# Optimization experiments

Measured on AMD Instinct MI355X. Metric: run time of the kernel, lower is better.

## Reference

```python
import jax, jax.numpy as jnp
import numpy as np

N_ROBOTS = 32   # len(cfg.ENV.WALKERS)
SEQ = 12        # cfg.MODEL.MAX_LIMBS
LOBS = 52       # per-limb proprioceptive obs size
HID = 256       # cfg.MODEL.MLP.HIDDEN_DIM
LOUT = 2        # out_dim // SEQ
BATCH = 1024


def _uniform(k, shape, r):
    return jax.random.uniform(k, shape, jnp.float32, -r, r)


def setup_inputs() -> dict:
    key = jax.random.key(0)
    ks = jax.random.split(key, 14)
    obs = jax.random.normal(ks[0], (BATCH, SEQ * LOBS), jnp.float32)
    obs_mask = jax.random.randint(ks[1], (BATCH, SEQ), 0, 2).astype(bool)
    unimal_ids = jax.random.randint(ks[2], (BATCH,), 0, N_ROBOTS).astype(jnp.int32)
    ir_in, ir = 0.04, 1.0 / 16
    return {
        "obs": obs,
        "obs_mask": obs_mask,
        "unimal_ids": unimal_ids,
        "Wi": _uniform(ks[3], (N_ROBOTS, SEQ, LOBS, HID), ir_in),
        "bi": _uniform(ks[4], (N_ROBOTS, SEQ, HID), ir_in / SEQ),
        "W1": _uniform(ks[5], (N_ROBOTS, HID, HID), ir),
        "b1": _uniform(ks[6], (N_ROBOTS, HID), ir),
        "W2": _uniform(ks[7], (N_ROBOTS, HID, HID), ir),
        "b2": _uniform(ks[8], (N_ROBOTS, HID), ir),
        "W3": _uniform(ks[9], (N_ROBOTS, HID, HID), ir),
        "b3": _uniform(ks[10], (N_ROBOTS, HID), ir),
        "Wo": _uniform(ks[11], (N_ROBOTS, SEQ, HID, LOUT), ir),
        "bo": _uniform(ks[12], (N_ROBOTS, SEQ, LOUT), ir),
    }


def reference(obs, obs_mask, unimal_ids, Wi, bi, W1, b1, W2, b2, W3, b3, Wo, bo):
    B = obs.shape[0]
    o3 = obs.reshape(B, SEQ, LOBS)
    # HN_INPUT branch: per-robot input hypernetwork weights
    emb = jnp.einsum("bsl,bslh->bsh", o3, Wi[unimal_ids]) + bi[unimal_ids]
    emb = emb * (1.0 - obs_mask.astype(emb.dtype))[:, :, None]
    emb = jax.nn.relu(emb.sum(axis=1))  # [B, HID]
    # PER_ROBOT_HIDDEN_LAYERS: three per-robot dense layers
    emb = jax.nn.relu(jnp.einsum("bh,bhk->bk", emb, W1[unimal_ids]) + b1[unimal_ids])
    emb = jax.nn.relu(jnp.einsum("bh,bhk->bk", emb, W2[unimal_ids]) + b2[unimal_ids])
    emb = jax.nn.relu(jnp.einsum("bh,bhk->bk", emb, W3[unimal_ids]) + b3[unimal_ids])
    # HN_OUTPUT branch: per-robot, per-limb output hypernetwork
    out = jnp.einsum("bh,bshd->bsd", emb, Wo[unimal_ids]) + bo[unimal_ids]
    return out.reshape(B, -1)  # [B, SEQ*LOUT]
```

## Files before the change

### kernel.cpp

```cpp
#include <hip/hip_runtime.h>

#define NROB 32
#define SEQ 12
#define LOBS 52
#define HID 256
#define LOUT 2
#define BATCH 1024
#define KIN 624
#define XROW 636
#define SPB 8
#define NSD 24
#define NBLK 320
#define SLOTS 40

__device__ __forceinline__ void fma4(float4& a, const float4 w, const float s) {
  a.x = fmaf(w.x, s, a.x);
  a.y = fmaf(w.y, s, a.y);
  a.z = fmaf(w.z, s, a.z);
  a.w = fmaf(w.w, s, a.w);
}

template <int ROWS, int XS>
__device__ __forceinline__ void stream8(const float* __restrict__ Wr,
                                        const float* Xb, float4* acc) {
  static_assert(ROWS % 8 == 0, "ROWS must be multiple of 8");
  constexpr int G = ROWS / 8;
  const float* wp = Wr;
  float4 a0 = *(const float4*)(wp);
  float4 a1 = *(const float4*)(wp + HID);
  float4 a2 = *(const float4*)(wp + 2 * HID);
  float4 a3 = *(const float4*)(wp + 3 * HID);
  wp += 4 * HID;
#pragma unroll
  for (int g = 0; g < G; ++g) {
    const int k = g * 8;
    const float4 b0 = *(const float4*)(wp);
    const float4 b1 = *(const float4*)(wp + HID);
    const float4 b2 = *(const float4*)(wp + 2 * HID);
    const float4 b3 = *(const float4*)(wp + 3 * HID);
    wp += 4 * HID;
#pragma unroll
    for (int m = 0; m < SPB; ++m) {
      const float4 x = *(const float4*)(Xb + m * XS + k);
      fma4(acc[m], a0, x.x);
      fma4(acc[m], a1, x.y);
      fma4(acc[m], a2, x.z);
      fma4(acc[m], a3, x.w);
    }
    if (g + 1 < G) {
      a0 = *(const float4*)(wp);
      a1 = *(const float4*)(wp + HID);
      a2 = *(const float4*)(wp + 2 * HID);
      a3 = *(const float4*)(wp + 3 * HID);
      wp += 4 * HID;
    }
#pragma unroll
    for (int m = 0; m < SPB; ++m) {
      const float4 x = *(const float4*)(Xb + m * XS + k + 4);
      fma4(acc[m], b0, x.x);
      fma4(acc[m], b1, x.y);
      fma4(acc[m], b2, x.z);
      fma4(acc[m], b3, x.w);
    }
  }
}

__global__ __launch_bounds__(512, 4) void k_fused(
    const float* __restrict__ obs, const int* __restrict__ mask,
    const int* __restrict__ ids, const float* __restrict__ Wi,
    const float* __restrict__ bi, const float* __restrict__ W1,
    const float* __restrict__ b1, const float* __restrict__ W2,
    const float* __restrict__ b2, const float* __restrict__ W3,
    const float* __restrict__ b3, const float* __restrict__ Wo,
    const float* __restrict__ bo, float* __restrict__ out) {
  __shared__ int s_cnt[NROB];
  __shared__ int s_wc[16];
  __shared__ int s_bm[SPB], s_vm[SPB], s_mb[SPB];
  __shared__ __align__(16) float s_x0[SPB * XROW];
  __shared__ __align__(16) float s_P[4][SPB][HID];
  __shared__ __align__(16) float s_x1[SPB][HID];

  const int t = threadIdx.x;
  const int bx = blockIdx.x;

  if (t < NROB) s_cnt[t] = 0;
  if (t < SPB) s_bm[t] = 0;
  __syncthreads();
  const int id0 = ids[t];
  const int id1 = ids[t + 512];
  atomicAdd(&s_cnt[id0], 1);
  atomicAdd(&s_cnt[id1], 1);
  __syncthreads();

  int myr = -1, mybase = 0;
  {
    int maxbucket = 0;
    for (int x = 0; x < 8; ++x) {
      int bsum = 0;
      for (int r = x; r < NROB; r += 8) bsum += (s_cnt[r] + SPB - 1) >> 3;
      maxbucket = max(maxbucket, bsum);
    }
    if (maxbucket <= SLOTS) {
      const int myxcd = bx & 7, myslot = bx >> 3;
      int slot = 0;
      for (int r = myxcd; r < NROB; r += 8) {
        const int nch = (s_cnt[r] + SPB - 1) >> 3;
        if (myr < 0 && myslot >= slot && myslot < slot + nch) {
          myr = r;
          mybase = (myslot - slot) * SPB;
        }
        slot += nch;
      }
    } else {
      int ch = 0;
      for (int r = 0; r < NROB; ++r) {
        const int nch = (s_cnt[r] + SPB - 1) >> 3;
        if (myr < 0 && bx >= ch && bx < ch + nch) {
          myr = r;
          mybase = (bx - ch) * SPB;
        }
        ch += nch;
      }
    }
  }
  if (myr < 0) return;
  const int mycnt = s_cnt[myr];

  {
    const int wv = t >> 6;
    const unsigned lane = t & 63;
    const unsigned long long m0 = __ballot(id0 == myr);
    const unsigned long long m1 = __ballot(id1 == myr);
    if (lane == 0) {
      s_wc[wv] = __popcll(m0);
      s_wc[8 + wv] = __popcll(m1);
    }
    __syncthreads();
    const unsigned long long below = (1ull << lane) - 1ull;
    int pre0 = 0;
    for (int i = 0; i < wv; ++i) pre0 += s_wc[i];
    if (id0 == myr) {
      const int j = pre0 + __popcll(m0 & below) - mybase;
      if (j >= 0 && j < SPB) s_bm[j] = t;
    }
    int pre1 = 0;
    for (int i = 0; i < 8 + wv; ++i) pre1 += s_wc[i];
    if (id1 == myr) {
      const int j = pre1 + __popcll(m1 & below) - mybase;
      if (j >= 0 && j < SPB) s_bm[j] = t + 512;
    }
    __syncthreads();
  }
  if (t < SPB) {
    const int v = (mybase + t) < mycnt;
    s_vm[t] = v;
    int mb = 0xFFF;
    if (v) {
      mb = 0;
      const int b = s_bm[t];
      for (int s = 0; s < SEQ; ++s) mb |= (mask[b * SEQ + s] != 0) << s;
    }
    s_mb[t] = mb;
  }
  __syncthreads();

  for (int q = t; q < SPB * (KIN / 4); q += 512) {
    const int m = q / 156, f4 = q - m * 156;
    const int s = f4 / 13;
    float4 v = {0.f, 0.f, 0.f, 0.f};
    if (!((s_mb[m] >> s) & 1))
      v = *(const float4*)(obs + (size_t)s_bm[m] * KIN + f4 * 4);
    *(float4*)&s_x0[m * XROW + f4 * 4] = v;
  }
  if (t < SPB * SEQ) {
    const int m = t / SEQ, s = t - m * SEQ;
    s_x0[m * XROW + KIN + s] = ((s_mb[m] >> s) & 1) ? 0.f : 1.f;
  }
  __syncthreads();

  const int w = t >> 6, lane = t & 63;

  {
    float4 acc[SPB];
#pragma unroll
    for (int m = 0; m < SPB; ++m) acc[m] = {0.f, 0.f, 0.f, 0.f};
    const float* Wr = Wi + ((size_t)myr * KIN + w * 80) * HID + lane * 4;
    if (w < 7)
      stream8<80, XROW>(Wr, &s_x0[w * 80], acc);
    else
      stream8<64, XROW>(Wr, &s_x0[w * 80], acc);
    float* Pp = &s_P[w >> 1][0][lane * 4];
    if ((w & 1) == 0) {
#pragma unroll
      for (int m = 0; m < SPB; ++m) *(float4*)(Pp + m * HID) = acc[m];
    }
    __syncthreads();
    if (w & 1) {
#pragma unroll
      for (int m = 0; m < SPB; ++m) {
        float4 c = *(const float4*)(Pp + m * HID);
        c.x += acc[m].x;
        c.y += acc[m].y;
        c.z += acc[m].z;
        c.w += acc[m].w;
        *(float4*)(Pp + m * HID) = c;
      }
    }
    __syncthreads();
    {
      const int m = t >> 6, c4 = (t & 63) * 4;
      const float4 p0 = *(const float4*)&s_P[0][m][c4];
      const float4 p1 = *(const float4*)&s_P[1][m][c4];
      const float4 p2 = *(const float4*)&s_P[2][m][c4];
      const float4 p3 = *(const float4*)&s_P[3][m][c4];
      float4 a = {p0.x + p1.x + p2.x + p3.x, p0.y + p1.y + p2.y + p3.y,
                  p0.z + p1.z + p2.z + p3.z, p0.w + p1.w + p2.w + p3.w};
      const float* br = bi + (size_t)myr * SEQ * HID + c4;
#pragma unroll
      for (int s = 0; s < SEQ; ++s)
        fma4(a, *(const float4*)(br + s * HID), s_x0[m * XROW + KIN + s]);
      float4 o = {fmaxf(a.x, 0.f), fmaxf(a.y, 0.f), fmaxf(a.z, 0.f),
                  fmaxf(a.w, 0.f)};
      *(float4*)&s_x1[m][c4] = o;
    }
    __syncthreads();
  }

  float* X2 = s_x0;
  const float* Ws[3] = {W1, W2, W3};
  const float* bs[3] = {b1, b2, b3};
#pragma unroll
  for (int L = 0; L < 3; ++L) {
    const float* Xin = (L & 1) ? X2 : &s_x1[0][0];
    float* Xout = (L & 1) ? &s_x1[0][0] : X2;
    float4 acc[SPB];
#pragma unroll
    for (int m = 0; m < SPB; ++m) acc[m] = {0.f, 0.f, 0.f, 0.f};
    const float* Wr = Ws[L] + ((size_t)myr * HID + w * 32) * HID + lane * 4;
    stream8<32, HID>(Wr, Xin + w * 32, acc);
    float* Pp = &s_P[w >> 1][0][lane * 4];
    if ((w & 1) == 0) {
#pragma unroll
      for (int m = 0; m < SPB; ++m) *(float4*)(Pp + m * HID) = acc[m];
    }
    __syncthreads();
    if (w & 1) {
#pragma unroll
      for (int m = 0; m < SPB; ++m) {
        float4 c = *(const float4*)(Pp + m * HID);
        c.x += acc[m].x;
        c.y += acc[m].y;
        c.z += acc[m].z;
        c.w += acc[m].w;
        *(float4*)(Pp + m * HID) = c;
      }
    }
    __syncthreads();
    {
      const int m = t >> 6, c4 = (t & 63) * 4;
      const float4 p0 = *(const float4*)&s_P[0][m][c4];
      const float4 p1 = *(const float4*)&s_P[1][m][c4];
      const float4 p2 = *(const float4*)&s_P[2][m][c4];
      const float4 p3 = *(const float4*)&s_P[3][m][c4];
      const float4 bv = *(const float4*)(bs[L] + (size_t)myr * HID + c4);
      float4 o = {fmaxf(p0.x + p1.x + p2.x + p3.x + bv.x, 0.f),
                  fmaxf(p0.y + p1.y + p2.y + p3.y + bv.y, 0.f),
                  fmaxf(p0.z + p1.z + p2.z + p3.z + bv.z, 0.f),
                  fmaxf(p0.w + p1.w + p2.w + p3.w + bv.w, 0.f)};
      *(float4*)(Xout + m * HID + c4) = o;
    }
    __syncthreads();
  }

  float* S = &s_P[0][0][0];
  {
    const float* Wop = Wo + (size_t)myr * SEQ * HID * LOUT;
    for (int q = t; q < (NSD * HID) / 4; q += 512) {
      const float4 v = *(const float4*)(Wop + q * 4);
      const int flat = q * 4;
      const int s = flat >> 9;
      const int k = (flat & 511) >> 1;
      S[(k + 0) * 25 + s * 2 + 0] = v.x;
      S[(k + 0) * 25 + s * 2 + 1] = v.y;
      S[(k + 1) * 25 + s * 2 + 0] = v.z;
      S[(k + 1) * 25 + s * 2 + 1] = v.w;
    }
  }
  __syncthreads();
  if (t < SPB * NSD) {
    const int m = t / NSD, sd = t - m * NSD;
    float a = bo[(size_t)myr * NSD + sd];
    const float* xp = X2 + m * HID;
#pragma unroll 8
    for (int k = 0; k < HID; ++k) a = fmaf(xp[k], S[k * 25 + sd], a);
    if (s_vm[m]) out[(size_t)s_bm[m] * NSD + sd] = a;
  }
}

extern "C" void kernel_launch(void* const* d_in, const int* in_sizes, int n_in,
                              void* d_out, int out_size, void* d_ws, size_t ws_size,
                              hipStream_t stream) {
  const float* obs = (const float*)d_in[0];
  const int* mask = (const int*)d_in[1];
  const int* ids = (const int*)d_in[2];
  const float* Wi = (const float*)d_in[3];
  const float* bi = (const float*)d_in[4];
  const float* W1 = (const float*)d_in[5];
  const float* b1 = (const float*)d_in[6];
  const float* W2 = (const float*)d_in[7];
  const float* b2 = (const float*)d_in[8];
  const float* W3 = (const float*)d_in[9];
  const float* b3 = (const float*)d_in[10];
  const float* Wo = (const float*)d_in[11];
  const float* bo = (const float*)d_in[12];
  float* out = (float*)d_out;
  (void)d_ws;
  hipLaunchKernelGGL(k_fused, dim3(NBLK), dim3(512), 0, stream, obs, mask, ids,
                     Wi, bi, W1, b1, W2, b2, W3, b3, Wo, bo, out);
}
```

Before: 41.10 us.

## Double block size to 1024 threads, splitting samples across wave pairs

Raises the block from 512 to 1024 threads. Each K-segment is now shared by two waves that each handle 4 of the 8 samples, so per-thread accumulators drop from 8 to 4 and there are twice as many waves to hide global weight-load latency. The stream loop now prefetches 8 weight rows at a time. Mask indicators move to a separate shared array, and each epilogue thread handles 2 columns instead of 4. In exchange, every block reads each weight row twice (once per sample half), and 1024-thread blocks may limit how many blocks fit per CU.

```diff
diff --git a/kernel.cpp b/kernel.cpp
--- a/kernel.cpp
+++ b/kernel.cpp
@@ -7,7 +7,6 @@
 #define LOUT 2
 #define BATCH 1024
 #define KIN 624
-#define XROW 636
 #define SPB 8
 #define NSD 24
 #define NBLK 320
@@ -20,52 +19,42 @@
   a.w = fmaf(w.w, s, a.w);
 }
 
-template <int ROWS, int XS>
-__device__ __forceinline__ void stream8(const float* __restrict__ Wr,
-                                        const float* Xb, float4* acc) {
-  static_assert(ROWS % 8 == 0, "ROWS must be multiple of 8");
+template <int ROWS, int SX>
+__device__ __forceinline__ void stream4(const float* __restrict__ wp,
+                                        const float* xb, float4* acc) {
+  static_assert(ROWS % 8 == 0, "ROWS multiple of 8");
   constexpr int G = ROWS / 8;
-  const float* wp = Wr;
-  float4 a0 = *(const float4*)(wp);
-  float4 a1 = *(const float4*)(wp + HID);
-  float4 a2 = *(const float4*)(wp + 2 * HID);
-  float4 a3 = *(const float4*)(wp + 3 * HID);
-  wp += 4 * HID;
+  float4 w[8];
+#pragma unroll
+  for (int j = 0; j < 8; ++j) w[j] = *(const float4*)(wp + j * HID);
+  wp += 8 * HID;
 #pragma unroll
   for (int g = 0; g < G; ++g) {
-    const int k = g * 8;
-    const float4 b0 = *(const float4*)(wp);
-    const float4 b1 = *(const float4*)(wp + HID);
-    const float4 b2 = *(const float4*)(wp + 2 * HID);
-    const float4 b3 = *(const float4*)(wp + 3 * HID);
-    wp += 4 * HID;
-#pragma unroll
-    for (int m = 0; m < SPB; ++m) {
-      const float4 x = *(const float4*)(Xb + m * XS + k);
-      fma4(acc[m], a0, x.x);
-      fma4(acc[m], a1, x.y);
-      fma4(acc[m], a2, x.z);
-      fma4(acc[m], a3, x.w);
-    }
+    float4 nw[8];
     if (g + 1 < G) {
-      a0 = *(const float4*)(wp);
-      a1 = *(const float4*)(wp + HID);
-      a2 = *(const float4*)(wp + 2 * HID);
-      a3 = *(const float4*)(wp + 3 * HID);
-      wp += 4 * HID;
-    }
-#pragma unroll
-    for (int m = 0; m < SPB; ++m) {
-      const float4 x = *(const float4*)(Xb + m * XS + k + 4);
-      fma4(acc[m], b0, x.x);
-      fma4(acc[m], b1, x.y);
-      fma4(acc[m], b2, x.z);
-      fma4(acc[m], b3, x.w);
-    }
+#pragma unroll
+      for (int j = 0; j < 8; ++j) nw[j] = *(const float4*)(wp + j * HID);
+      wp += 8 * HID;
+    }
+#pragma unroll
+    for (int i = 0; i < 4; ++i) {
+      const float4 xa = *(const float4*)(xb + i * SX + g * 8);
+      const float4 xc = *(const float4*)(xb + i * SX + g * 8 + 4);
+      fma4(acc[i], w[0], xa.x);
+      fma4(acc[i], w[1], xa.y);
+      fma4(acc[i], w[2], xa.z);
+      fma4(acc[i], w[3], xa.w);
+      fma4(acc[i], w[4], xc.x);
+      fma4(acc[i], w[5], xc.y);
+      fma4(acc[i], w[6], xc.z);
+      fma4(acc[i], w[7], xc.w);
+    }
+#pragma unroll
+    for (int j = 0; j < 8; ++j) w[j] = nw[j];
   }
 }
 
-__global__ __launch_bounds__(512, 4) void k_fused(
+__global__ __launch_bounds__(1024, 4) void k_fused(
     const float* __restrict__ obs, const int* __restrict__ mask,
     const int* __restrict__ ids, const float* __restrict__ Wi,
     const float* __restrict__ bi, const float* __restrict__ W1,
@@ -76,7 +65,8 @@
   __shared__ int s_cnt[NROB];
   __shared__ int s_wc[16];
   __shared__ int s_bm[SPB], s_vm[SPB], s_mb[SPB];
-  __shared__ __align__(16) float s_x0[SPB * XROW];
+  __shared__ float s_ind[SPB][SEQ];
+  __shared__ __align__(16) float s_x0[SPB * KIN];
   __shared__ __align__(16) float s_P[4][SPB][HID];
   __shared__ __align__(16) float s_x1[SPB][HID];
 
@@ -87,9 +77,7 @@
   if (t < SPB) s_bm[t] = 0;
   __syncthreads();
   const int id0 = ids[t];
-  const int id1 = ids[t + 512];
   atomicAdd(&s_cnt[id0], 1);
-  atomicAdd(&s_cnt[id1], 1);
   __syncthreads();
 
   int myr = -1, mybase = 0;
@@ -130,24 +118,14 @@
     const int wv = t >> 6;
     const unsigned lane = t & 63;
     const unsigned long long m0 = __ballot(id0 == myr);
-    const unsigned long long m1 = __ballot(id1 == myr);
-    if (lane == 0) {
-      s_wc[wv] = __popcll(m0);
-      s_wc[8 + wv] = __popcll(m1);
-    }
-    __syncthreads();
-    const unsigned long long below = (1ull << lane) - 1ull;
-    int pre0 = 0;
-    for (int i = 0; i < wv; ++i) pre0 += s_wc[i];
+    if (lane == 0) s_wc[wv] = __popcll(m0);
+    __syncthreads();
+    int pre = 0;
+    for (int i = 0; i < wv; ++i) pre += s_wc[i];
     if (id0 == myr) {
-      const int j = pre0 + __popcll(m0 & below) - mybase;
+      const unsigned long long below = (1ull << lane) - 1ull;
+      const int j = pre + __popcll(m0 & below) - mybase;
       if (j >= 0 && j < SPB) s_bm[j] = t;
-    }
-    int pre1 = 0;
-    for (int i = 0; i < 8 + wv; ++i) pre1 += s_wc[i];
-    if (id1 == myr) {
-      const int j = pre1 + __popcll(m1 & below) - mybase;
-      if (j >= 0 && j < SPB) s_bm[j] = t + 512;
     }
     __syncthreads();
   }
@@ -162,66 +140,73 @@
     }
     s_mb[t] = mb;
   }
-  __syncthreads();
-
-  for (int q = t; q < SPB * (KIN / 4); q += 512) {
+  if (t >= 64 && t < 64 + SPB * SEQ) {
+  }
+  __syncthreads();
+  if (t < SPB * SEQ) {
+    const int m = t / SEQ, s = t - m * SEQ;
+    s_ind[m][s] = ((s_mb[m] >> s) & 1) ? 0.f : 1.f;
+  }
+  for (int q = t; q < SPB * (KIN / 4); q += 1024) {
     const int m = q / 156, f4 = q - m * 156;
     const int s = f4 / 13;
     float4 v = {0.f, 0.f, 0.f, 0.f};
     if (!((s_mb[m] >> s) & 1))
       v = *(const float4*)(obs + (size_t)s_bm[m] * KIN + f4 * 4);
-    *(float4*)&s_x0[m * XROW + f4 * 4] = v;
-  }
-  if (t < SPB * SEQ) {
-    const int m = t / SEQ, s = t - m * SEQ;
-    s_x0[m * XROW + KIN + s] = ((s_mb[m] >> s) & 1) ? 0.f : 1.f;
+    *(float4*)&s_x0[m * KIN + f4 * 4] = v;
   }
   __syncthreads();
 
   const int w = t >> 6, lane = t & 63;
+  const int seg = w >> 1, sg = w & 1;
+  float* Pp = &s_P[seg & 3][sg * 4][lane * 4];
 
   {
-    float4 acc[SPB];
-#pragma unroll
-    for (int m = 0; m < SPB; ++m) acc[m] = {0.f, 0.f, 0.f, 0.f};
-    const float* Wr = Wi + ((size_t)myr * KIN + w * 80) * HID + lane * 4;
-    if (w < 7)
-      stream8<80, XROW>(Wr, &s_x0[w * 80], acc);
+    float4 acc[4];
+#pragma unroll
+    for (int i = 0; i < 4; ++i) acc[i] = {0.f, 0.f, 0.f, 0.f};
+    const float* Wr = Wi + ((size_t)myr * KIN + seg * 80) * HID + lane * 4;
+    const float* xb = &s_x0[(sg * 4) * KIN + seg * 80];
+    if (seg < 7)
+      stream4<80, KIN>(Wr, xb, acc);
     else
-      stream8<64, XROW>(Wr, &s_x0[w * 80], acc);
-    float* Pp = &s_P[w >> 1][0][lane * 4];
-    if ((w & 1) == 0) {
-#pragma unroll
-      for (int m = 0; m < SPB; ++m) *(float4*)(Pp + m * HID) = acc[m];
-    }
-    __syncthreads();
-    if (w & 1) {
-#pragma unroll
-      for (int m = 0; m < SPB; ++m) {
-        float4 c = *(const float4*)(Pp + m * HID);
-        c.x += acc[m].x;
-        c.y += acc[m].y;
-        c.z += acc[m].z;
-        c.w += acc[m].w;
-        *(float4*)(Pp + m * HID) = c;
+      stream4<64, KIN>(Wr, xb, acc);
+    if (seg < 4) {
+#pragma unroll
+      for (int i = 0; i < 4; ++i) *(float4*)(Pp + i * HID) = acc[i];
+    }
+    __syncthreads();
+    if (seg >= 4) {
+#pragma unroll
+      for (int i = 0; i < 4; ++i) {
+        float4 c = *(const float4*)(Pp + i * HID);
+        c.x += acc[i].x;
+        c.y += acc[i].y;
+        c.z += acc[i].z;
+        c.w += acc[i].w;
+        *(float4*)(Pp + i * HID) = c;
       }
     }
     __syncthreads();
     {
-      const int m = t >> 6, c4 = (t & 63) * 4;
-      const float4 p0 = *(const float4*)&s_P[0][m][c4];
-      const float4 p1 = *(const float4*)&s_P[1][m][c4];
-      const float4 p2 = *(const float4*)&s_P[2][m][c4];
-      const float4 p3 = *(const float4*)&s_P[3][m][c4];
-      float4 a = {p0.x + p1.x + p2.x + p3.x, p0.y + p1.y + p2.y + p3.y,
-                  p0.z + p1.z + p2.z + p3.z, p0.w + p1.w + p2.w + p3.w};
-      const float* br = bi + (size_t)myr * SEQ * HID + c4;
-#pragma unroll
-      for (int s = 0; s < SEQ; ++s)
-        fma4(a, *(const float4*)(br + s * HID), s_x0[m * XROW + KIN + s]);
-      float4 o = {fmaxf(a.x, 0.f), fmaxf(a.y, 0.f), fmaxf(a.z, 0.f),
-                  fmaxf(a.w, 0.f)};
-      *(float4*)&s_x1[m][c4] = o;
+      const int m = t >> 7, c2 = (t & 127) * 2;
+      float2 a = {0.f, 0.f};
+#pragma unroll
+      for (int j = 0; j < 4; ++j) {
+        const float2 p = *(const float2*)&s_P[j][m][c2];
+        a.x += p.x;
+        a.y += p.y;
+      }
+      const float* br = bi + (size_t)myr * SEQ * HID + c2;
+#pragma unroll
+      for (int s = 0; s < SEQ; ++s) {
+        const float2 b2v = *(const float2*)(br + s * HID);
+        const float f = s_ind[m][s];
+        a.x = fmaf(b2v.x, f, a.x);
+        a.y = fmaf(b2v.y, f, a.y);
+      }
+      s_x1[m][c2] = fmaxf(a.x, 0.f);
+      s_x1[m][c2 + 1] = fmaxf(a.y, 0.f);
     }
     __syncthreads();
   }
@@ -233,41 +218,40 @@
   for (int L = 0; L < 3; ++L) {
     const float* Xin = (L & 1) ? X2 : &s_x1[0][0];
     float* Xout = (L & 1) ? &s_x1[0][0] : X2;
-    float4 acc[SPB];
-#pragma unroll
-    for (int m = 0; m < SPB; ++m) acc[m] = {0.f, 0.f, 0.f, 0.f};
-    const float* Wr = Ws[L] + ((size_t)myr * HID + w * 32) * HID + lane * 4;
-    stream8<32, HID>(Wr, Xin + w * 32, acc);
-    float* Pp = &s_P[w >> 1][0][lane * 4];
-    if ((w & 1) == 0) {
-#pragma unroll
-      for (int m = 0; m < SPB; ++m) *(float4*)(Pp + m * HID) = acc[m];
-    }
-    __syncthreads();
-    if (w & 1) {
-#pragma unroll
-      for (int m = 0; m < SPB; ++m) {
-        float4 c = *(const float4*)(Pp + m * HID);
-        c.x += acc[m].x;
-        c.y += acc[m].y;
-        c.z += acc[m].z;
-        c.w += acc[m].w;
-        *(float4*)(Pp + m * HID) = c;
+    float4 acc[4];
+#pragma unroll
+    for (int i = 0; i < 4; ++i) acc[i] = {0.f, 0.f, 0.f, 0.f};
+    const float* Wr = Ws[L] + ((size_t)myr * HID + seg * 32) * HID + lane * 4;
+    stream4<32, HID>(Wr, Xin + (sg * 4) * HID + seg * 32, acc);
+    if (seg < 4) {
+#pragma unroll
+      for (int i = 0; i < 4; ++i) *(float4*)(Pp + i * HID) = acc[i];
+    }
+    __syncthreads();
+    if (seg >= 4) {
+#pragma unroll
+      for (int i = 0; i < 4; ++i) {
+        float4 c = *(const float4*)(Pp + i * HID);
+        c.x += acc[i].x;
+        c.y += acc[i].y;
+        c.z += acc[i].z;
+        c.w += acc[i].w;
+        *(float4*)(Pp + i * HID) = c;
       }
     }
     __syncthreads();
     {
-      const int m = t >> 6, c4 = (t & 63) * 4;
-      const float4 p0 = *(const float4*)&s_P[0][m][c4];
-      const float4 p1 = *(const float4*)&s_P[1][m][c4];
-      const float4 p2 = *(const float4*)&s_P[2][m][c4];
-      const float4 p3 = *(const float4*)&s_P[3][m][c4];
-      const float4 bv = *(const float4*)(bs[L] + (size_t)myr * HID + c4);
-      float4 o = {fmaxf(p0.x + p1.x + p2.x + p3.x + bv.x, 0.f),
-                  fmaxf(p0.y + p1.y + p2.y + p3.y + bv.y, 0.f),
-                  fmaxf(p0.z + p1.z + p2.z + p3.z + bv.z, 0.f),
-                  fmaxf(p0.w + p1.w + p2.w + p3.w + bv.w, 0.f)};
-      *(float4*)(Xout + m * HID + c4) = o;
+      const int m = t >> 7, c2 = (t & 127) * 2;
+      float2 a = {0.f, 0.f};
+#pragma unroll
+      for (int j = 0; j < 4; ++j) {
+        const float2 p = *(const float2*)&s_P[j][m][c2];
+        a.x += p.x;
+        a.y += p.y;
+      }
+      const float2 bv = *(const float2*)(bs[L] + (size_t)myr * HID + c2);
+      Xout[m * HID + c2] = fmaxf(a.x + bv.x, 0.f);
+      Xout[m * HID + c2 + 1] = fmaxf(a.y + bv.y, 0.f);
     }
     __syncthreads();
   }
@@ -275,7 +259,7 @@
   float* S = &s_P[0][0][0];
   {
     const float* Wop = Wo + (size_t)myr * SEQ * HID * LOUT;
-    for (int q = t; q < (NSD * HID) / 4; q += 512) {
+    for (int q = t; q < (NSD * HID) / 4; q += 1024) {
       const float4 v = *(const float4*)(Wop + q * 4);
       const int flat = q * 4;
       const int s = flat >> 9;
@@ -315,6 +299,6 @@
   const float* bo = (const float*)d_in[12];
   float* out = (float*)d_out;
   (void)d_ws;
-  hipLaunchKernelGGL(k_fused, dim3(NBLK), dim3(512), 0, stream, obs, mask, ids,
+  hipLaunchKernelGGL(k_fused, dim3(NBLK), dim3(1024), 0, stream, obs, mask, ids,
                      Wi, bi, W1, b1, W2, b2, W3, b3, Wo, bo, out);
 }
```

Result: no change. 40.35 us (-1.8%).
